# Kernel tuning notes

Hardware: AMD Instinct MI355X
Metric: run time of the kernel (lower is better)

## Reference

```python
import jax, jax.numpy as jnp
import numpy as np
import math

B, S, H, L, N, V = 4, 2048, 1024, 4, 4, 256
D = H // N
EPS = 1e-5


def setup_inputs() -> dict:
    key = jax.random.key(0)
    ks = iter(jax.random.split(key, 40))
    sc = 1.0 / math.sqrt(H)
    def w(shape, s=None):
        return jax.random.normal(next(ks), shape, dtype=jnp.float32) * (s if s is not None else sc)
    inp = {
        "input_ids": jax.random.randint(next(ks), (B, S), 0, V, dtype=jnp.int32),
        "embed": w((V, H), 0.02),
        "nm_gate_w": w((H, H)), "nm_gate_b": jnp.zeros((H,), jnp.float32),
        "nm_filter_w": w((H, H)), "nm_filter_b": jnp.zeros((H,), jnp.float32),
        "nm_ctx_w": w((2, H)), "nm_ctx_b": jnp.zeros((2,), jnp.float32),
        "q_w": w((L, H, H)), "q_b": jnp.zeros((L, H), jnp.float32),
        "k_w": w((L, H, H)), "k_b": jnp.zeros((L, H), jnp.float32),
        "v_w": w((L, H, H)), "v_b": jnp.zeros((L, H), jnp.float32),
        "gain_w": w((L, N, H)), "gain_b": jnp.zeros((L, N), jnp.float32),
        "attn_ow": w((L, H, H)), "attn_ob": jnp.zeros((L, H), jnp.float32),
        "en_w": w((L, H, H)), "en_b": jnp.zeros((L, H), jnp.float32),
        "plastic_w": w((L, H, H)),
        "fix_w": w((L, H, H)), "fix_b": jnp.zeros((L, H), jnp.float32),
        "ln_g": jnp.ones((L, H), jnp.float32), "ln_b": jnp.zeros((L, H), jnp.float32),
        "out_w": w((V, H)), "out_b": jnp.zeros((V,), jnp.float32),
    }
    return inp


def _forward(input_ids, embed, nm_gate_w, nm_gate_b, nm_filter_w, nm_filter_b,
             nm_ctx_w, nm_ctx_b, q_w, q_b, k_w, k_b, v_w, v_b, gain_w, gain_b,
             attn_ow, attn_ob, en_w, en_b, plastic_w, fix_w, fix_b, ln_g, ln_b,
             out_w, out_b):
    x = embed[input_ids]                                   # [B,S,H]
    # --- NeurotransmitterModule ---
    ctx = x.mean(axis=1)                                   # [B,H]
    nm = ctx @ nm_ctx_w.T + nm_ctx_b                       # [B,2]
    dop, nor = nm[:, :1], nm[:, 1:]                        # [B,1] each
    gate = jax.nn.sigmoid(x @ nm_gate_w.T + nm_gate_b)
    x = x * (1.0 + dop[:, None, :] * gate)
    noise = jnp.tanh(x @ nm_filter_w.T + nm_filter_b)
    x = x + nor[:, None, :] * noise
    inv_sqrt_d = 1.0 / math.sqrt(D)
    for l in range(L):
        # --- GainControlAttention ---
        q = (x @ q_w[l].T + q_b[l]).reshape(B, S, N, D).transpose(0, 2, 1, 3)
        k = (x @ k_w[l].T + k_b[l]).reshape(B, S, N, D).transpose(0, 2, 1, 3)
        v = (x @ v_w[l].T + v_b[l]).reshape(B, S, N, D).transpose(0, 2, 1, 3)
        gain = x.mean(axis=1) @ gain_w[l].T + gain_b[l]    # [B,N]
        q = q * (1.0 + gain[:, :, None, None])
        scores = jnp.einsum('bnsd,bntd->bnst', q, k) * inv_sqrt_d
        attn = jax.nn.softmax(scores, axis=-1)
        ctxv = jnp.einsum('bnst,bntd->bnsd', attn, v)
        a = ctxv.transpose(0, 2, 1, 3).reshape(B, S, H) @ attn_ow[l].T + attn_ob[l]
        x = x + a
        # --- EnergyConstrainedLayer ---
        x = jax.nn.silu(x @ en_w[l].T + en_b[l])
        # --- NeuroplasticityLayer (eval mode) ---
        x = x + (x @ fix_w[l].T + fix_b[l]) + (x @ plastic_w[l].T)
        # --- LayerNorm ---
        mu = x.mean(axis=-1, keepdims=True)
        var = jnp.mean((x - mu) ** 2, axis=-1, keepdims=True)
        x = (x - mu) * jax.lax.rsqrt(var + EPS) * ln_g[l] + ln_b[l]
    return x @ out_w.T + out_b                             # [B,S,V]


def reference(input_ids, embed, nm_gate_w, nm_gate_b, nm_filter_w, nm_filter_b,
              nm_ctx_w, nm_ctx_b, q_w, q_b, k_w, k_b, v_w, v_b, gain_w, gain_b,
              attn_ow, attn_ob, en_w, en_b, plastic_w, fix_w, fix_b, ln_g, ln_b,
              out_w, out_b):
    return _forward(input_ids, embed, nm_gate_w, nm_gate_b, nm_filter_w,
                    nm_filter_b, nm_ctx_w, nm_ctx_b, q_w, q_b, k_w, k_b, v_w,
                    v_b, gain_w, gain_b, attn_ow, attn_ob, en_w, en_b,
                    plastic_w, fix_w, fix_b, ln_g, ln_b, out_w, out_b)
```

## Files before the change

kernel.cpp:

```cpp
#include <hip/hip_runtime.h>

#define B_ 4
#define S_ 2048
#define H_ 1024
#define L_ 4
#define N_ 4
#define D_ 256
#define V_ 256
#define EPSF 1e-5f

typedef __attribute__((ext_vector_type(8))) short short8;
typedef __attribute__((ext_vector_type(4))) float f32x4;

__device__ inline float bf2f(unsigned short u) {
    union { unsigned int ui; float f; } c; c.ui = ((unsigned int)u) << 16; return c.f;
}
__device__ inline unsigned short f2bf(float f) {
    union { float f; unsigned int ui; } c; c.f = f;
    unsigned int u = c.ui;
    unsigned int r = (u + 0x7FFFu + ((u >> 16) & 1u)) >> 16;
    return (unsigned short)r;
}
__device__ inline float wave64_sum(float v) {
    for (int m = 32; m >= 1; m >>= 1) v += __shfl_xor(v, m, 64);
    return v;
}
__device__ inline void gl_lds16(const unsigned short* g, unsigned short* l) {
    __builtin_amdgcn_global_load_lds(
        (const __attribute__((address_space(1))) unsigned int*)g,
        (__attribute__((address_space(3))) unsigned int*)l, 16, 0, 0);
}

__global__ void wcvt_kernel(const float* __restrict__ W,
                            unsigned short* __restrict__ Wb, int n8) {
    int idx = blockIdx.x * 256 + threadIdx.x;
    if (idx >= n8) return;
    size_t base = (size_t)idx * 8;
    float4 a0 = *(const float4*)(W + base);
    float4 a1 = *(const float4*)(W + base + 4);
    short8 t;
    t[0] = f2bf(a0.x); t[1] = f2bf(a0.y); t[2] = f2bf(a0.z); t[3] = f2bf(a0.w);
    t[4] = f2bf(a1.x); t[5] = f2bf(a1.y); t[6] = f2bf(a1.z); t[7] = f2bf(a1.w);
    *(short8*)(Wb + base) = t;
}

__global__ void wadd_kernel(const float* __restrict__ Wa, const float* __restrict__ Wb2,
                            unsigned short* __restrict__ Wo, int n8) {
    int idx = blockIdx.x * 256 + threadIdx.x;
    if (idx >= n8) return;
    size_t base = (size_t)idx * 8;
    short8 t;
#pragma unroll
    for (int e = 0; e < 8; e++) {
        size_t p = base + e;
        int pos = (int)(p & ((size_t)H_ * H_ - 1));
        float v = Wa[p] + Wb2[p] + (((pos >> 10) == (pos & (H_ - 1))) ? 1.f : 0.f);
        t[e] = f2bf(v);
    }
    *(short8*)(Wo + base) = t;
}

__global__ void gather_kernel(const int* __restrict__ ids,
                              const float* __restrict__ embed,
                              unsigned short* __restrict__ x) {
    size_t idx = (size_t)blockIdx.x * 256 + threadIdx.x;
    int bs = (int)(idx >> 10);
    int h  = (int)(idx & 1023);
    x[idx] = f2bf(embed[(size_t)ids[bs] * H_ + h]);
}

__global__ void mean_kernel(const unsigned short* __restrict__ Xin,
                            float* __restrict__ xmean) {
    int idx = blockIdx.x * 256 + threadIdx.x;
    int b = idx >> 10, h = idx & 1023;
    int s0 = blockIdx.y * 128;
    const unsigned short* p = Xin + ((size_t)b * S_ + s0) * H_ + h;
    float s = 0.f;
    for (int i = 0; i < 128; i++) s += bf2f(p[(size_t)i * H_]);
    atomicAdd(&xmean[idx], s);
}

__global__ void nm_kernel(const float* __restrict__ xmean,
                          const float* __restrict__ w,
                          const float* __restrict__ bias,
                          float* __restrict__ dopnor) {
    int wave = threadIdx.x >> 6, lane = threadIdx.x & 63;
    for (int p = wave; p < 2 * B_; p += 4) {
        int b = p >> 1, j = p & 1;
        float s = 0.f;
        for (int h = lane; h < H_; h += 64) s += xmean[b * H_ + h] * w[j * H_ + h];
        s = wave64_sum(s);
        if (lane == 0) dopnor[p] = s / (float)S_ + bias[j];
    }
}

__global__ void gain_kernel(const float* __restrict__ xmean,
                            const float* __restrict__ gw,
                            const float* __restrict__ gb,
                            float* __restrict__ qscale) {
    int wave = threadIdx.x >> 6, lane = threadIdx.x & 63;
    for (int p = wave; p < B_ * N_; p += 4) {
        int b = p >> 2, n = p & 3;
        float s = 0.f;
        for (int h = lane; h < H_; h += 64) s += xmean[b * H_ + h] * gw[n * H_ + h];
        s = wave64_sum(s);
        if (lane == 0) qscale[p] = (1.f + s / (float)S_ + gb[n]) * 0.0625f;
    }
}

__global__ __launch_bounds__(256) void gemm_bt(
    const unsigned short* __restrict__ A, const unsigned short* __restrict__ W,
    const float* __restrict__ bias, void* __restrict__ Cout,
    const unsigned short* __restrict__ X, const float* __restrict__ scal,
    int K, int Nout, int mode) {
    __shared__ unsigned short As[128 * 32];
    __shared__ unsigned short Bs[128 * 32];
    int tid = threadIdx.x;
    int wave = tid >> 6, lane = tid & 63;
    int quad = lane >> 4, l16 = lane & 15;
    int bm = blockIdx.x * 128;
    int bn = blockIdx.y * 128;
    int mw = (wave >> 1) * 64, nw = (wave & 1) * 64;

    const unsigned short* Ag = A + (size_t)(bm + wave * 16 + (lane >> 2)) * K + (lane & 3) * 8;
    const unsigned short* Wg = W + (size_t)(bn + wave * 16 + (lane >> 2)) * K + (lane & 3) * 8;
    unsigned short* ldsA = As + wave * 512;
    unsigned short* ldsB = Bs + wave * 512;
    size_t rowskip = (size_t)64 * K;

    f32x4 acc[4][4];
#pragma unroll
    for (int i = 0; i < 4; i++)
#pragma unroll
        for (int j = 0; j < 4; j++)
#pragma unroll
            for (int r = 0; r < 4; r++) acc[i][j][r] = 0.f;

    for (int kk = 0; kk < K; kk += 32) {
        __syncthreads();
        gl_lds16(Ag + kk, ldsA);
        gl_lds16(Ag + rowskip + kk, ldsA + 2048);
        gl_lds16(Wg + kk, ldsB);
        gl_lds16(Wg + rowskip + kk, ldsB + 2048);
        __syncthreads();

        short8 af[4], bfr[4];
#pragma unroll
        for (int i = 0; i < 4; i++)
            af[i] = *(const short8*)&As[(mw + i * 16 + l16) * 32 + quad * 8];
#pragma unroll
        for (int j = 0; j < 4; j++)
            bfr[j] = *(const short8*)&Bs[(nw + j * 16 + l16) * 32 + quad * 8];
#pragma unroll
        for (int i = 0; i < 4; i++)
#pragma unroll
            for (int j = 0; j < 4; j++)
                acc[i][j] = __builtin_amdgcn_mfma_f32_16x16x32_bf16(af[i], bfr[j], acc[i][j], 0, 0, 0);
    }

    if (mode == 6) {
#pragma unroll
        for (int i = 0; i < 4; i++) {
#pragma unroll
            for (int j = 0; j < 4; j++) {
                int col = bn + nw + j * 16 + l16;
                float bv = bias ? bias[col] : 0.f;
                int n = col >> 8, d = col & 255;
                int row0 = bm + mw + i * 16 + quad * 4;
                int b = row0 >> 11, s0 = row0 & 2047;
                union { unsigned short u[4]; uint2 v; } pk;
#pragma unroll
                for (int r = 0; r < 4; r++) pk.u[r] = f2bf(acc[i][j][r] + bv);
                *(uint2*)((unsigned short*)Cout +
                          ((size_t)(b * N_ + n) * D_ + d) * S_ + s0) = pk.v;
            }
        }
        return;
    }

#pragma unroll
    for (int i = 0; i < 4; i++) {
#pragma unroll
        for (int j = 0; j < 4; j++) {
            int col = bn + nw + j * 16 + l16;
            float bv = bias ? bias[col] : 0.f;
#pragma unroll
            for (int r = 0; r < 4; r++) {
                int row = bm + mw + i * 16 + quad * 4 + r;
                float v = acc[i][j][r] + bv;
                size_t off = (size_t)row * Nout + col;
                if (mode == 5) {
                    ((float*)Cout)[off] = v;
                    continue;
                }
                float outv;
                if (mode == 0) {
                    outv = v;
                } else if (mode == 1) {
                    float sig = 1.f / (1.f + __expf(-v));
                    float dop = scal[(row >> 11) * 2];
                    outv = bf2f(X[off]) * (1.f + dop * sig);
                } else if (mode == 2) {
                    float nor = scal[(row >> 11) * 2 + 1];
                    outv = bf2f(X[off]) + nor * tanhf(v);
                } else if (mode == 3) {
                    outv = v + bf2f(X[off]);
                } else {
                    outv = v * (1.f / (1.f + __expf(-v)));
                }
                ((unsigned short*)Cout)[off] = f2bf(outv);
            }
        }
    }
}

__global__ __launch_bounds__(512) void flash_attn(
    const unsigned short* __restrict__ Q, const unsigned short* __restrict__ Kg,
    const unsigned short* __restrict__ VT, const float* __restrict__ qscale,
    unsigned short* __restrict__ O) {
    __shared__ unsigned short Kt[64][264];
    __shared__ unsigned short Vtl[272][72];
    __shared__ unsigned short Pl[8][16][72];

    int tid = threadIdx.x;
    int wave = tid >> 6, lane = tid & 63;
    int quad = lane >> 4, l16 = lane & 15;
    int bnh = blockIdx.y;
    size_t base = ((size_t)(bnh >> 2) * S_) * H_ + (size_t)(bnh & 3) * D_;
    size_t vtbase = (size_t)bnh * D_ * S_;
    int qw = blockIdx.x * 128 + wave * 16;
    float scale = qscale[bnh];

    for (int c = tid; c < 16 * 72; c += 512) {
        int rr = c / 72, cc = c - rr * 72;
        Vtl[256 + rr][cc] = (rr == 0) ? (unsigned short)0x3F80 : (unsigned short)0;
    }

    short8 qf[8];
#pragma unroll
    for (int kk = 0; kk < 8; kk++)
        qf[kk] = *(const short8*)(Q + base + (size_t)(qw + l16) * H_ + kk * 32 + quad * 8);

    f32x4 o[16], osum;
#pragma unroll
    for (int c = 0; c < 16; c++)
#pragma unroll
        for (int r = 0; r < 4; r++) o[c][r] = 0.f;
#pragma unroll
    for (int r = 0; r < 4; r++) osum[r] = 0.f;
    float mrow[4] = {-1e30f, -1e30f, -1e30f, -1e30f};

    for (int t0 = 0; t0 < S_; t0 += 64) {
        __syncthreads();
#pragma unroll
        for (int rr = 0; rr < 4; rr++) {
            int c = rr * 512 + tid;
            int row = c >> 5, col = (c & 31) * 8;
            *(short8*)&Kt[row][col] =
                *(const short8*)(Kg + base + (size_t)(t0 + row) * H_ + col);
        }
#pragma unroll
        for (int rr = 0; rr < 4; rr++) {
            int c = rr * 512 + tid;
            int d = c >> 3, col = (c & 7) * 8;
            *(short8*)&Vtl[d][col] =
                *(const short8*)(VT + vtbase + (size_t)d * S_ + t0 + col);
        }
        __syncthreads();

        f32x4 s[4];
#pragma unroll
        for (int j = 0; j < 4; j++)
#pragma unroll
            for (int r = 0; r < 4; r++) s[j][r] = 0.f;
#pragma unroll
        for (int j = 0; j < 4; j++)
#pragma unroll
            for (int kk = 0; kk < 8; kk++) {
                short8 kf = *(const short8*)&Kt[j * 16 + l16][kk * 32 + quad * 8];
                s[j] = __builtin_amdgcn_mfma_f32_16x16x32_bf16(qf[kk], kf, s[j], 0, 0, 0);
            }

        float alpha[4];
#pragma unroll
        for (int r = 0; r < 4; r++) {
            float sv[4];
#pragma unroll
            for (int j = 0; j < 4; j++) sv[j] = s[j][r] * scale;
            float mx = fmaxf(fmaxf(sv[0], sv[1]), fmaxf(sv[2], sv[3]));
            for (int m = 8; m >= 1; m >>= 1) mx = fmaxf(mx, __shfl_xor(mx, m, 64));
            float mnew = fmaxf(mrow[r], mx);
            alpha[r] = __expf(mrow[r] - mnew);
            mrow[r] = mnew;
#pragma unroll
            for (int j = 0; j < 4; j++)
                Pl[wave][quad * 4 + r][j * 16 + l16] = f2bf(__expf(sv[j] - mnew));
        }
#pragma unroll
        for (int c = 0; c < 16; c++)
#pragma unroll
            for (int r = 0; r < 4; r++) o[c][r] *= alpha[r];
#pragma unroll
        for (int r = 0; r < 4; r++) osum[r] *= alpha[r];

        short8 pf0 = *(const short8*)&Pl[wave][l16][quad * 8];
        short8 pf1 = *(const short8*)&Pl[wave][l16][32 + quad * 8];
#pragma unroll
        for (int c = 0; c < 16; c++) {
            short8 vf0 = *(const short8*)&Vtl[c * 16 + l16][quad * 8];
            o[c] = __builtin_amdgcn_mfma_f32_16x16x32_bf16(pf0, vf0, o[c], 0, 0, 0);
            short8 vf1 = *(const short8*)&Vtl[c * 16 + l16][32 + quad * 8];
            o[c] = __builtin_amdgcn_mfma_f32_16x16x32_bf16(pf1, vf1, o[c], 0, 0, 0);
        }
        {
            short8 vs0 = *(const short8*)&Vtl[256 + l16][quad * 8];
            osum = __builtin_amdgcn_mfma_f32_16x16x32_bf16(pf0, vs0, osum, 0, 0, 0);
            short8 vs1 = *(const short8*)&Vtl[256 + l16][32 + quad * 8];
            osum = __builtin_amdgcn_mfma_f32_16x16x32_bf16(pf1, vs1, osum, 0, 0, 0);
        }
    }

    float invl[4];
#pragma unroll
    for (int r = 0; r < 4; r++)
        invl[r] = 1.f / __shfl(osum[r], (lane & 48), 64);
#pragma unroll
    for (int c = 0; c < 16; c++)
#pragma unroll
        for (int r = 0; r < 4; r++) {
            int row = qw + quad * 4 + r;
            int d = c * 16 + l16;
            O[base + (size_t)row * H_ + d] = f2bf(o[c][r] * invl[r]);
        }
}

__global__ __launch_bounds__(256) void ln_kernel(
    const unsigned short* __restrict__ y, const float* __restrict__ g,
    const float* __restrict__ bta, unsigned short* __restrict__ out) {
    int row = blockIdx.x;
    size_t ro = (size_t)row * H_;
    int tid = threadIdx.x;
    float t[4]; float s = 0.f, s2 = 0.f;
#pragma unroll
    for (int i = 0; i < 4; i++) {
        int h = i * 256 + tid;
        float v = bf2f(y[ro + h]);
        t[i] = v; s += v; s2 += v * v;
    }
    s = wave64_sum(s); s2 = wave64_sum(s2);
    __shared__ float sh[8];
    int wave = tid >> 6, lane = tid & 63;
    if (lane == 0) { sh[wave] = s; sh[4 + wave] = s2; }
    __syncthreads();
    s  = sh[0] + sh[1] + sh[2] + sh[3];
    s2 = sh[4] + sh[5] + sh[6] + sh[7];
    float mu = s * (1.f / H_);
    float var = s2 * (1.f / H_) - mu * mu;
    float inv = rsqrtf(var + EPSF);
#pragma unroll
    for (int i = 0; i < 4; i++) {
        int h = i * 256 + tid;
        out[ro + h] = f2bf((t[i] - mu) * inv * g[h] + bta[h]);
    }
}

extern "C" void kernel_launch(void* const* d_in, const int* in_sizes, int n_in,
                              void* d_out, int out_size, void* d_ws, size_t ws_size,
                              hipStream_t stream) {
    const int*   ids          = (const int*)d_in[0];
    const float* embed        = (const float*)d_in[1];
    const float* nm_gate_w    = (const float*)d_in[2];
    const float* nm_gate_b    = (const float*)d_in[3];
    const float* nm_filter_w  = (const float*)d_in[4];
    const float* nm_filter_b  = (const float*)d_in[5];
    const float* nm_ctx_w     = (const float*)d_in[6];
    const float* nm_ctx_b     = (const float*)d_in[7];
    const float* q_w          = (const float*)d_in[8];
    const float* q_b          = (const float*)d_in[9];
    const float* k_w          = (const float*)d_in[10];
    const float* k_b          = (const float*)d_in[11];
    const float* v_w          = (const float*)d_in[12];
    const float* v_b          = (const float*)d_in[13];
    const float* gain_w       = (const float*)d_in[14];
    const float* gain_b       = (const float*)d_in[15];
    const float* attn_ow      = (const float*)d_in[16];
    const float* attn_ob      = (const float*)d_in[17];
    const float* en_w         = (const float*)d_in[18];
    const float* en_b         = (const float*)d_in[19];
    const float* plastic_w    = (const float*)d_in[20];
    const float* fix_w        = (const float*)d_in[21];
    const float* fix_b        = (const float*)d_in[22];
    const float* ln_g         = (const float*)d_in[23];
    const float* ln_b         = (const float*)d_in[24];
    const float* out_w        = (const float*)d_in[25];
    const float* out_b        = (const float*)d_in[26];

    size_t T  = (size_t)B_ * S_ * H_;
    size_t WH = (size_t)H_ * H_;
    size_t smallBytes = ((size_t)B_ * H_ + 2 * B_ + B_ * N_ + 8) * sizeof(float);
    size_t megaElems  = 26 * WH + WH / 4;
    size_t need_base  = 4 * T * 2 + smallBytes + 2 * WH;
    size_t need_mega  = 4 * T * 2 + smallBytes + 2 * megaElems;
    if (ws_size < need_base) return;
    bool mega = ws_size >= need_mega;

    unsigned short* X   = (unsigned short*)d_ws;
    unsigned short* Qb  = X + T;
    unsigned short* Kb  = Qb + T;
    unsigned short* Vb  = Kb + T;
    float* xmean  = (float*)(Vb + T);
    float* dopnor = xmean + (size_t)B_ * H_;
    float* qscale = dopnor + 2 * B_;
    unsigned short* Wbase = (unsigned short*)(qscale + B_ * N_ + 8);
#define WOFF(k) (Wbase + (size_t)(k) * WH)

    const int M   = B_ * S_;
    const int W8  = (int)(WH / 8);
    const int WG  = (W8 + 255) / 256;
    const int W84 = (int)(4 * WH / 8);
    const int WG4 = (W84 + 255) / 256;
    const int W8o = V_ * H_ / 8;
    const int WGo = (W8o + 255) / 256;

    if (mega) {
        wcvt_kernel<<<WG,  256, 0, stream>>>(nm_gate_w,   WOFF(0),  W8);
        wcvt_kernel<<<WG,  256, 0, stream>>>(nm_filter_w, WOFF(1),  W8);
        wcvt_kernel<<<WG4, 256, 0, stream>>>(q_w,         WOFF(2),  W84);
        wcvt_kernel<<<WG4, 256, 0, stream>>>(k_w,         WOFF(6),  W84);
        wcvt_kernel<<<WG4, 256, 0, stream>>>(v_w,         WOFF(10), W84);
        wcvt_kernel<<<WG4, 256, 0, stream>>>(attn_ow,     WOFF(14), W84);
        wcvt_kernel<<<WG4, 256, 0, stream>>>(en_w,        WOFF(18), W84);
        wadd_kernel<<<WG4, 256, 0, stream>>>(fix_w, plastic_w, WOFF(22), W84);
        wcvt_kernel<<<WGo, 256, 0, stream>>>(out_w,       WOFF(26), W8o);
    }

    gather_kernel<<<dim3((int)(T / 256)), 256, 0, stream>>>(ids, embed, X);

    hipMemsetAsync(xmean, 0, (size_t)B_ * H_ * sizeof(float), stream);
    mean_kernel<<<dim3(B_ * H_ / 256, 16), 256, 0, stream>>>(X, xmean);
    nm_kernel<<<1, 256, 0, stream>>>(xmean, nm_ctx_w, nm_ctx_b, dopnor);

    const unsigned short* Wp;
    if (mega) Wp = WOFF(0);
    else { wcvt_kernel<<<WG, 256, 0, stream>>>(nm_gate_w, Wbase, W8); Wp = Wbase; }
    gemm_bt<<<dim3(M / 128, H_ / 128), 256, 0, stream>>>(
        X, Wp, nm_gate_b, Qb, X, dopnor, H_, H_, 1);
    if (mega) Wp = WOFF(1);
    else { wcvt_kernel<<<WG, 256, 0, stream>>>(nm_filter_w, Wbase, W8); Wp = Wbase; }
    gemm_bt<<<dim3(M / 128, H_ / 128), 256, 0, stream>>>(
        Qb, Wp, nm_filter_b, X, Qb, dopnor, H_, H_, 2);

    for (int l = 0; l < L_; l++) {
        size_t wo = (size_t)l * WH;
        size_t bo = (size_t)l * H_;
        hipMemsetAsync(xmean, 0, (size_t)B_ * H_ * sizeof(float), stream);
        mean_kernel<<<dim3(B_ * H_ / 256, 16), 256, 0, stream>>>(X, xmean);
        gain_kernel<<<1, 256, 0, stream>>>(xmean, gain_w + (size_t)l * N_ * H_,
                                           gain_b + (size_t)l * N_, qscale);

        if (mega) Wp = WOFF(2) + wo;
        else { wcvt_kernel<<<WG, 256, 0, stream>>>(q_w + wo, Wbase, W8); Wp = Wbase; }
        gemm_bt<<<dim3(M / 128, H_ / 128), 256, 0, stream>>>(
            X, Wp, q_b + bo, Qb, nullptr, nullptr, H_, H_, 0);
        if (mega) Wp = WOFF(6) + wo;
        else { wcvt_kernel<<<WG, 256, 0, stream>>>(k_w + wo, Wbase, W8); Wp = Wbase; }
        gemm_bt<<<dim3(M / 128, H_ / 128), 256, 0, stream>>>(
            X, Wp, k_b + bo, Kb, nullptr, nullptr, H_, H_, 0);
        if (mega) Wp = WOFF(10) + wo;
        else { wcvt_kernel<<<WG, 256, 0, stream>>>(v_w + wo, Wbase, W8); Wp = Wbase; }
        gemm_bt<<<dim3(M / 128, H_ / 128), 256, 0, stream>>>(
            X, Wp, v_b + bo, Vb, nullptr, nullptr, H_, H_, 6);

        flash_attn<<<dim3(S_ / 128, B_ * N_), 512, 0, stream>>>(Qb, Kb, Vb, qscale, Qb);

        if (mega) Wp = WOFF(14) + wo;
        else { wcvt_kernel<<<WG, 256, 0, stream>>>(attn_ow + wo, Wbase, W8); Wp = Wbase; }
        gemm_bt<<<dim3(M / 128, H_ / 128), 256, 0, stream>>>(
            Qb, Wp, attn_ob + bo, Kb, X, nullptr, H_, H_, 3);
        if (mega) Wp = WOFF(18) + wo;
        else { wcvt_kernel<<<WG, 256, 0, stream>>>(en_w + wo, Wbase, W8); Wp = Wbase; }
        gemm_bt<<<dim3(M / 128, H_ / 128), 256, 0, stream>>>(
            Kb, Wp, en_b + bo, Vb, nullptr, nullptr, H_, H_, 4);
        if (mega) Wp = WOFF(22) + wo;
        else { wadd_kernel<<<WG, 256, 0, stream>>>(fix_w + wo, plastic_w + wo, Wbase, W8); Wp = Wbase; }
        gemm_bt<<<dim3(M / 128, H_ / 128), 256, 0, stream>>>(
            Vb, Wp, fix_b + bo, Qb, nullptr, nullptr, H_, H_, 0);
        ln_kernel<<<dim3(M), 256, 0, stream>>>(Qb, ln_g + bo, ln_b + bo, X);
    }

    if (mega) Wp = WOFF(26);
    else { wcvt_kernel<<<WGo, 256, 0, stream>>>(out_w, Wbase, W8o); Wp = Wbase; }
    gemm_bt<<<dim3(M / 128, V_ / 128), 256, 0, stream>>>(
        X, Wp, out_b, (float*)d_out, nullptr, nullptr, H_, V_, 5);
#undef WOFF
}
```

Baseline: 1.924 ms.

## Fuse QKV projections into one GEMM and split attention over key halves

Q, K and V weights are interleaved per layer so a single GEMM launch with a 3x wider N grid produces all three outputs, with V written transposed in the epilogue. Attention is split into two key-range halves, each processing 32 query rows per wave, and a merge kernel combines the partial outputs using the stored row max and sum. The split doubles the attention grid along the key axis and raises per-wave reuse of K/V tiles, at the cost of writing and re-reading two extra full-size partial buffers plus extra workspace. Both paths depend on the workspace being large enough.

Result: slower. 2.271 ms (+18.0%).

```diff
diff --git a/kernel.cpp b/kernel.cpp
--- a/kernel.cpp
+++ b/kernel.cpp
@@ -8,6 +8,7 @@
 #define D_ 256
 #define V_ 256
 #define EPSF 1e-5f
+#define WH_ ((size_t)H_ * H_)
 
 typedef __attribute__((ext_vector_type(8))) short short8;
 typedef __attribute__((ext_vector_type(4))) float f32x4;
@@ -44,6 +45,22 @@
     *(short8*)(Wb + base) = t;
 }
 
+__global__ void wcvt_qkv(const float* __restrict__ W,
+                         unsigned short* __restrict__ Wb, int n8, int sel) {
+    int idx = blockIdx.x * 256 + threadIdx.x;
+    if (idx >= n8) return;
+    size_t p = (size_t)idx * 8;
+    size_t layer = p >> 20;
+    size_t within = p & (WH_ - 1);
+    size_t dst = layer * 3 * WH_ + (size_t)sel * WH_ + within;
+    float4 a0 = *(const float4*)(W + p);
+    float4 a1 = *(const float4*)(W + p + 4);
+    short8 t;
+    t[0] = f2bf(a0.x); t[1] = f2bf(a0.y); t[2] = f2bf(a0.z); t[3] = f2bf(a0.w);
+    t[4] = f2bf(a1.x); t[5] = f2bf(a1.y); t[6] = f2bf(a1.z); t[7] = f2bf(a1.w);
+    *(short8*)(Wb + dst) = t;
+}
+
 __global__ void wadd_kernel(const float* __restrict__ Wa, const float* __restrict__ Wb2,
                             unsigned short* __restrict__ Wo, int n8) {
     int idx = blockIdx.x * 256 + threadIdx.x;
@@ -53,7 +70,7 @@
 #pragma unroll
     for (int e = 0; e < 8; e++) {
         size_t p = base + e;
-        int pos = (int)(p & ((size_t)H_ * H_ - 1));
+        int pos = (int)(p & (WH_ - 1));
         float v = Wa[p] + Wb2[p] + (((pos >> 10) == (pos & (H_ - 1))) ? 1.f : 0.f);
         t[e] = f2bf(v);
     }
@@ -214,6 +231,93 @@
     }
 }
 
+__global__ __launch_bounds__(256) void gemm_qkv(
+    const unsigned short* __restrict__ A, const unsigned short* __restrict__ W,
+    const float* __restrict__ qb, const float* __restrict__ kb,
+    const float* __restrict__ vbb, unsigned short* __restrict__ Qo,
+    unsigned short* __restrict__ Ko, unsigned short* __restrict__ Vt) {
+    __shared__ unsigned short As[128 * 32];
+    __shared__ unsigned short Bs[128 * 32];
+    const int K = H_;
+    int tid = threadIdx.x;
+    int wave = tid >> 6, lane = tid & 63;
+    int quad = lane >> 4, l16 = lane & 15;
+    int bm = blockIdx.x * 128;
+    int bn = blockIdx.y * 128;
+    int mw = (wave >> 1) * 64, nw = (wave & 1) * 64;
+
+    const unsigned short* Ag = A + (size_t)(bm + wave * 16 + (lane >> 2)) * K + (lane & 3) * 8;
+    const unsigned short* Wg = W + (size_t)(bn + wave * 16 + (lane >> 2)) * K + (lane & 3) * 8;
+    unsigned short* ldsA = As + wave * 512;
+    unsigned short* ldsB = Bs + wave * 512;
+    size_t rowskip = (size_t)64 * K;
+
+    f32x4 acc[4][4];
+#pragma unroll
+    for (int i = 0; i < 4; i++)
+#pragma unroll
+        for (int j = 0; j < 4; j++)
+#pragma unroll
+            for (int r = 0; r < 4; r++) acc[i][j][r] = 0.f;
+
+    for (int kk = 0; kk < K; kk += 32) {
+        __syncthreads();
+        gl_lds16(Ag + kk, ldsA);
+        gl_lds16(Ag + rowskip + kk, ldsA + 2048);
+        gl_lds16(Wg + kk, ldsB);
+        gl_lds16(Wg + rowskip + kk, ldsB + 2048);
+        __syncthreads();
+
+        short8 af[4], bfr[4];
+#pragma unroll
+        for (int i = 0; i < 4; i++)
+            af[i] = *(const short8*)&As[(mw + i * 16 + l16) * 32 + quad * 8];
+#pragma unroll
+        for (int j = 0; j < 4; j++)
+            bfr[j] = *(const short8*)&Bs[(nw + j * 16 + l16) * 32 + quad * 8];
+#pragma unroll
+        for (int i = 0; i < 4; i++)
+#pragma unroll
+            for (int j = 0; j < 4; j++)
+                acc[i][j] = __builtin_amdgcn_mfma_f32_16x16x32_bf16(af[i], bfr[j], acc[i][j], 0, 0, 0);
+    }
+
+    int sel = (bn + nw) >> 10;
+    if (sel == 2) {
+#pragma unroll
+        for (int i = 0; i < 4; i++) {
+#pragma unroll
+            for (int j = 0; j < 4; j++) {
+                int c2 = ((bn + nw) & 1023) + j * 16 + l16;
+                float bv = vbb[c2];
+                int n = c2 >> 8, d = c2 & 255;
+                int row0 = bm + mw + i * 16 + quad * 4;
+                int b = row0 >> 11, s0 = row0 & 2047;
+                union { unsigned short u[4]; uint2 v; } pk;
+#pragma unroll
+                for (int r = 0; r < 4; r++) pk.u[r] = f2bf(acc[i][j][r] + bv);
+                *(uint2*)(Vt + ((size_t)(b * N_ + n) * D_ + d) * S_ + s0) = pk.v;
+            }
+        }
+    } else {
+        unsigned short* Co = (sel == 0) ? Qo : Ko;
+        const float* bias = (sel == 0) ? qb : kb;
+#pragma unroll
+        for (int i = 0; i < 4; i++) {
+#pragma unroll
+            for (int j = 0; j < 4; j++) {
+                int c2 = ((bn + nw) & 1023) + j * 16 + l16;
+                float bv = bias[c2];
+#pragma unroll
+                for (int r = 0; r < 4; r++) {
+                    int row = bm + mw + i * 16 + quad * 4 + r;
+                    Co[(size_t)row * H_ + c2] = f2bf(acc[i][j][r] + bv);
+                }
+            }
+        }
+    }
+}
+
 __global__ __launch_bounds__(512) void flash_attn(
     const unsigned short* __restrict__ Q, const unsigned short* __restrict__ Kg,
     const unsigned short* __restrict__ VT, const float* __restrict__ qscale,
@@ -332,6 +436,189 @@
             int d = c * 16 + l16;
             O[base + (size_t)row * H_ + d] = f2bf(o[c][r] * invl[r]);
         }
+}
+
+__global__ __launch_bounds__(512) void flash_split(
+    const unsigned short* __restrict__ Q, const unsigned short* __restrict__ Kg,
+    const unsigned short* __restrict__ VT, const float* __restrict__ qscale,
+    unsigned short* __restrict__ Pout, float2* __restrict__ ml) {
+    __shared__ unsigned short Kt[64][264];
+    __shared__ unsigned short Vtl[272][72];
+    __shared__ unsigned short Pl[8][32][72];
+
+    int tid = threadIdx.x;
+    int wave = tid >> 6, lane = tid & 63;
+    int quad = lane >> 4, l16 = lane & 15;
+    int bnh = blockIdx.z;
+    int half = blockIdx.y;
+    size_t base = ((size_t)(bnh >> 2) * S_) * H_ + (size_t)(bnh & 3) * D_;
+    size_t vtbase = (size_t)bnh * D_ * S_;
+    int qw = blockIdx.x * 256 + wave * 32;
+    float scale = qscale[bnh];
+    unsigned short* Ph = Pout + (size_t)half * B_ * S_ * H_;
+
+    for (int c = tid; c < 16 * 72; c += 512) {
+        int rr = c / 72, cc = c - rr * 72;
+        Vtl[256 + rr][cc] = (rr == 0) ? (unsigned short)0x3F80 : (unsigned short)0;
+    }
+
+    short8 qf[2][8];
+#pragma unroll
+    for (int rt = 0; rt < 2; rt++)
+#pragma unroll
+        for (int kk = 0; kk < 8; kk++)
+            qf[rt][kk] = *(const short8*)(Q + base +
+                (size_t)(qw + rt * 16 + l16) * H_ + kk * 32 + quad * 8);
+
+    f32x4 o[2][16], osum[2];
+#pragma unroll
+    for (int rt = 0; rt < 2; rt++) {
+#pragma unroll
+        for (int c = 0; c < 16; c++)
+#pragma unroll
+            for (int r = 0; r < 4; r++) o[rt][c][r] = 0.f;
+#pragma unroll
+        for (int r = 0; r < 4; r++) osum[rt][r] = 0.f;
+    }
+    float mrow[2][4];
+#pragma unroll
+    for (int rt = 0; rt < 2; rt++)
+#pragma unroll
+        for (int r = 0; r < 4; r++) mrow[rt][r] = -1e30f;
+
+    int tbeg = half * (S_ / 2);
+    for (int tt = 0; tt < S_ / 2; tt += 64) {
+        int t0 = tbeg + tt;
+        __syncthreads();
+#pragma unroll
+        for (int rr = 0; rr < 4; rr++) {
+            int c = rr * 512 + tid;
+            int row = c >> 5, col = (c & 31) * 8;
+            *(short8*)&Kt[row][col] =
+                *(const short8*)(Kg + base + (size_t)(t0 + row) * H_ + col);
+        }
+#pragma unroll
+        for (int rr = 0; rr < 4; rr++) {
+            int c = rr * 512 + tid;
+            int d = c >> 3, col = (c & 7) * 8;
+            *(short8*)&Vtl[d][col] =
+                *(const short8*)(VT + vtbase + (size_t)d * S_ + t0 + col);
+        }
+        __syncthreads();
+
+        f32x4 s0[4], s1[4];
+#pragma unroll
+        for (int j = 0; j < 4; j++)
+#pragma unroll
+            for (int r = 0; r < 4; r++) { s0[j][r] = 0.f; s1[j][r] = 0.f; }
+#pragma unroll
+        for (int j = 0; j < 4; j++)
+#pragma unroll
+            for (int kk = 0; kk < 8; kk++) {
+                short8 kf = *(const short8*)&Kt[j * 16 + l16][kk * 32 + quad * 8];
+                s0[j] = __builtin_amdgcn_mfma_f32_16x16x32_bf16(qf[0][kk], kf, s0[j], 0, 0, 0);
+                s1[j] = __builtin_amdgcn_mfma_f32_16x16x32_bf16(qf[1][kk], kf, s1[j], 0, 0, 0);
+            }
+
+#pragma unroll
+        for (int rt = 0; rt < 2; rt++) {
+            float alpha[4];
+#pragma unroll
+            for (int r = 0; r < 4; r++) {
+                float sv[4];
+#pragma unroll
+                for (int j = 0; j < 4; j++)
+                    sv[j] = (rt == 0 ? s0[j][r] : s1[j][r]) * scale;
+                float mx = fmaxf(fmaxf(sv[0], sv[1]), fmaxf(sv[2], sv[3]));
+                for (int m = 8; m >= 1; m >>= 1) mx = fmaxf(mx, __shfl_xor(mx, m, 64));
+                float mnew = fmaxf(mrow[rt][r], mx);
+                alpha[r] = __expf(mrow[rt][r] - mnew);
+                mrow[rt][r] = mnew;
+#pragma unroll
+                for (int j = 0; j < 4; j++)
+                    Pl[wave][rt * 16 + quad * 4 + r][j * 16 + l16] =
+                        f2bf(__expf(sv[j] - mnew));
+            }
+#pragma unroll
+            for (int c = 0; c < 16; c++)
+#pragma unroll
+                for (int r = 0; r < 4; r++) o[rt][c][r] *= alpha[r];
+#pragma unroll
+            for (int r = 0; r < 4; r++) osum[rt][r] *= alpha[r];
+        }
+
+        short8 pf[2][2];
+#pragma unroll
+        for (int rt = 0; rt < 2; rt++) {
+            pf[rt][0] = *(const short8*)&Pl[wave][rt * 16 + l16][quad * 8];
+            pf[rt][1] = *(const short8*)&Pl[wave][rt * 16 + l16][32 + quad * 8];
+        }
+#pragma unroll
+        for (int c = 0; c < 16; c++) {
+            short8 vf0 = *(const short8*)&Vtl[c * 16 + l16][quad * 8];
+            o[0][c] = __builtin_amdgcn_mfma_f32_16x16x32_bf16(pf[0][0], vf0, o[0][c], 0, 0, 0);
+            o[1][c] = __builtin_amdgcn_mfma_f32_16x16x32_bf16(pf[1][0], vf0, o[1][c], 0, 0, 0);
+            short8 vf1 = *(const short8*)&Vtl[c * 16 + l16][32 + quad * 8];
+            o[0][c] = __builtin_amdgcn_mfma_f32_16x16x32_bf16(pf[0][1], vf1, o[0][c], 0, 0, 0);
+            o[1][c] = __builtin_amdgcn_mfma_f32_16x16x32_bf16(pf[1][1], vf1, o[1][c], 0, 0, 0);
+        }
+        {
+            short8 vs0 = *(const short8*)&Vtl[256 + l16][quad * 8];
+            short8 vs1 = *(const short8*)&Vtl[256 + l16][32 + quad * 8];
+            osum[0] = __builtin_amdgcn_mfma_f32_16x16x32_bf16(pf[0][0], vs0, osum[0], 0, 0, 0);
+            osum[0] = __builtin_amdgcn_mfma_f32_16x16x32_bf16(pf[0][1], vs1, osum[0], 0, 0, 0);
+            osum[1] = __builtin_amdgcn_mfma_f32_16x16x32_bf16(pf[1][0], vs0, osum[1], 0, 0, 0);
+            osum[1] = __builtin_amdgcn_mfma_f32_16x16x32_bf16(pf[1][1], vs1, osum[1], 0, 0, 0);
+        }
+    }
+
+#pragma unroll
+    for (int rt = 0; rt < 2; rt++) {
+        float invl[4];
+#pragma unroll
+        for (int r = 0; r < 4; r++)
+            invl[r] = 1.f / __shfl(osum[rt][r], (lane & 48), 64);
+        if (l16 == 0) {
+#pragma unroll
+            for (int r = 0; r < 4; r++) {
+                int row = qw + rt * 16 + quad * 4 + r;
+                float2 v; v.x = mrow[rt][r]; v.y = osum[rt][r];
+                ml[((size_t)half * 16 + bnh) * S_ + row] = v;
+            }
+        }
+#pragma unroll
+        for (int c = 0; c < 16; c++)
+#pragma unroll
+            for (int r = 0; r < 4; r++) {
+                int row = qw + rt * 16 + quad * 4 + r;
+                int d = c * 16 + l16;
+                Ph[base + (size_t)row * H_ + d] = f2bf(o[rt][c][r] * invl[r]);
+            }
+    }
+}
+
+__global__ __launch_bounds__(256) void flash_merge(
+    const unsigned short* __restrict__ P1, const unsigned short* __restrict__ P2,
+    const float2* __restrict__ ml, unsigned short* __restrict__ O) {
+    size_t e = ((size_t)blockIdx.x * 256 + threadIdx.x) * 8;
+    int grow = (int)(e >> 10);
+    int h0 = (int)(e & 1023);
+    int b = grow >> 11, s = grow & 2047;
+    int bnh = b * N_ + (h0 >> 8);
+    float2 a = ml[(size_t)bnh * S_ + s];
+    float2 c = ml[((size_t)16 + bnh) * S_ + s];
+    float m = fmaxf(a.x, c.x);
+    float w1 = a.y * __expf(a.x - m);
+    float w2 = c.y * __expf(c.x - m);
+    float inv = 1.f / (w1 + w2);
+    w1 *= inv; w2 *= inv;
+    short8 x1 = *(const short8*)(P1 + e);
+    short8 x2 = *(const short8*)(P2 + e);
+    short8 t;
+#pragma unroll
+    for (int i = 0; i < 8; i++)
+        t[i] = f2bf(w1 * bf2f((unsigned short)x1[i]) + w2 * bf2f((unsigned short)x2[i]));
+    *(short8*)(O + e) = t;
 }
 
 __global__ __launch_bounds__(256) void ln_kernel(
@@ -396,13 +683,15 @@
     const float* out_b        = (const float*)d_in[26];
 
     size_t T  = (size_t)B_ * S_ * H_;
-    size_t WH = (size_t)H_ * H_;
     size_t smallBytes = ((size_t)B_ * H_ + 2 * B_ + B_ * N_ + 8) * sizeof(float);
-    size_t megaElems  = 26 * WH + WH / 4;
-    size_t need_base  = 4 * T * 2 + smallBytes + 2 * WH;
+    size_t megaElems  = 26 * WH_ + WH_ / 4;
+    size_t mlBytes    = (size_t)2 * 16 * S_ * sizeof(float2);
+    size_t need_base  = 4 * T * 2 + smallBytes + 2 * WH_;
     size_t need_mega  = 4 * T * 2 + smallBytes + 2 * megaElems;
+    size_t need_split = need_mega + 2 * T * 2 + mlBytes;
     if (ws_size < need_base) return;
-    bool mega = ws_size >= need_mega;
+    bool mega  = ws_size >= need_mega;
+    bool split = ws_size >= need_split;
 
     unsigned short* X   = (unsigned short*)d_ws;
     unsigned short* Qb  = X + T;
@@ -412,26 +701,28 @@
     float* dopnor = xmean + (size_t)B_ * H_;
     float* qscale = dopnor + 2 * B_;
     unsigned short* Wbase = (unsigned short*)(qscale + B_ * N_ + 8);
-#define WOFF(k) (Wbase + (size_t)(k) * WH)
+    unsigned short* Pbuf  = Wbase + megaElems;
+    float2* mlbuf = (float2*)(Pbuf + 2 * T);
+#define WOFF(k) (Wbase + (size_t)(k) * WH_)
 
     const int M   = B_ * S_;
-    const int W8  = (int)(WH / 8);
+    const int W8  = (int)(WH_ / 8);
     const int WG  = (W8 + 255) / 256;
-    const int W84 = (int)(4 * WH / 8);
+    const int W84 = (int)(4 * WH_ / 8);
     const int WG4 = (W84 + 255) / 256;
     const int W8o = V_ * H_ / 8;
     const int WGo = (W8o + 255) / 256;
 
     if (mega) {
-        wcvt_kernel<<<WG,  256, 0, stream>>>(nm_gate_w,   WOFF(0),  W8);
-        wcvt_kernel<<<WG,  256, 0, stream>>>(nm_filter_w, WOFF(1),  W8);
-        wcvt_kernel<<<WG4, 256, 0, stream>>>(q_w,         WOFF(2),  W84);
-        wcvt_kernel<<<WG4, 256, 0, stream>>>(k_w,         WOFF(6),  W84);
-        wcvt_kernel<<<WG4, 256, 0, stream>>>(v_w,         WOFF(10), W84);
-        wcvt_kernel<<<WG4, 256, 0, stream>>>(attn_ow,     WOFF(14), W84);
-        wcvt_kernel<<<WG4, 256, 0, stream>>>(en_w,        WOFF(18), W84);
+        wcvt_kernel<<<WG,  256, 0, stream>>>(nm_gate_w,   WOFF(0), W8);
+        wcvt_kernel<<<WG,  256, 0, stream>>>(nm_filter_w, WOFF(1), W8);
+        wcvt_qkv<<<WG4, 256, 0, stream>>>(q_w, WOFF(2), W84, 0);
+        wcvt_qkv<<<WG4, 256, 0, stream>>>(k_w, WOFF(2), W84, 1);
+        wcvt_qkv<<<WG4, 256, 0, stream>>>(v_w, WOFF(2), W84, 2);
+        wcvt_kernel<<<WG4, 256, 0, stream>>>(attn_ow, WOFF(14), W84);
+        wcvt_kernel<<<WG4, 256, 0, stream>>>(en_w,    WOFF(18), W84);
         wadd_kernel<<<WG4, 256, 0, stream>>>(fix_w, plastic_w, WOFF(22), W84);
-        wcvt_kernel<<<WGo, 256, 0, stream>>>(out_w,       WOFF(26), W8o);
+        wcvt_kernel<<<WGo, 256, 0, stream>>>(out_w, WOFF(26), W8o);
     }
 
     gather_kernel<<<dim3((int)(T / 256)), 256, 0, stream>>>(ids, embed, X);
@@ -451,27 +742,38 @@
         Qb, Wp, nm_filter_b, X, Qb, dopnor, H_, H_, 2);
 
     for (int l = 0; l < L_; l++) {
-        size_t wo = (size_t)l * WH;
+        size_t wo = (size_t)l * WH_;
         size_t bo = (size_t)l * H_;
         hipMemsetAsync(xmean, 0, (size_t)B_ * H_ * sizeof(float), stream);
         mean_kernel<<<dim3(B_ * H_ / 256, 16), 256, 0, stream>>>(X, xmean);
         gain_kernel<<<1, 256, 0, stream>>>(xmean, gain_w + (size_t)l * N_ * H_,
                                            gain_b + (size_t)l * N_, qscale);
 
-        if (mega) Wp = WOFF(2) + wo;
-        else { wcvt_kernel<<<WG, 256, 0, stream>>>(q_w + wo, Wbase, W8); Wp = Wbase; }
-        gemm_bt<<<dim3(M / 128, H_ / 128), 256, 0, stream>>>(
-            X, Wp, q_b + bo, Qb, nullptr, nullptr, H_, H_, 0);
-        if (mega) Wp = WOFF(6) + wo;
-        else { wcvt_kernel<<<WG, 256, 0, stream>>>(k_w + wo, Wbase, W8); Wp = Wbase; }
-        gemm_bt<<<dim3(M / 128, H_ / 128), 256, 0, stream>>>(
-            X, Wp, k_b + bo, Kb, nullptr, nullptr, H_, H_, 0);
-        if (mega) Wp = WOFF(10) + wo;
-        else { wcvt_kernel<<<WG, 256, 0, stream>>>(v_w + wo, Wbase, W8); Wp = Wbase; }
-        gemm_bt<<<dim3(M / 128, H_ / 128), 256, 0, stream>>>(
-            X, Wp, v_b + bo, Vb, nullptr, nullptr, H_, H_, 6);
-
-        flash_attn<<<dim3(S_ / 128, B_ * N_), 512, 0, stream>>>(Qb, Kb, Vb, qscale, Qb);
+        if (mega) {
+            gemm_qkv<<<dim3(M / 128, 3 * H_ / 128), 256, 0, stream>>>(
+                X, WOFF(2) + (size_t)l * 3 * WH_, q_b + bo, k_b + bo, v_b + bo,
+                Qb, Kb, Vb);
+        } else {
+            wcvt_kernel<<<WG, 256, 0, stream>>>(q_w + wo, Wbase, W8);
+            gemm_bt<<<dim3(M / 128, H_ / 128), 256, 0, stream>>>(
+                X, Wbase, q_b + bo, Qb, nullptr, nullptr, H_, H_, 0);
+            wcvt_kernel<<<WG, 256, 0, stream>>>(k_w + wo, Wbase, W8);
+            gemm_bt<<<dim3(M / 128, H_ / 128), 256, 0, stream>>>(
+                X, Wbase, k_b + bo, Kb, nullptr, nullptr, H_, H_, 0);
+            wcvt_kernel<<<WG, 256, 0, stream>>>(v_w + wo, Wbase, W8);
+            gemm_bt<<<dim3(M / 128, H_ / 128), 256, 0, stream>>>(
+                X, Wbase, v_b + bo, Vb, nullptr, nullptr, H_, H_, 6);
+        }
+
+        if (split) {
+            flash_split<<<dim3(S_ / 256, 2, B_ * N_), 512, 0, stream>>>(
+                Qb, Kb, Vb, qscale, Pbuf, mlbuf);
+            flash_merge<<<dim3((int)(T / 8 / 256)), 256, 0, stream>>>(
+                Pbuf, Pbuf + T, mlbuf, Qb);
+        } else {
+            flash_attn<<<dim3(S_ / 128, B_ * N_), 512, 0, stream>>>(
+                Qb, Kb, Vb, qscale, Qb);
+        }
 
         if (mega) Wp = WOFF(14) + wo;
         else { wcvt_kernel<<<WG, 256, 0, stream>>>(attn_ow + wo, Wbase, W8); Wp = Wbase; }
```
